# Performance work log

Measured on AMD Instinct MI355X. Metric: run time of the kernel, lower is better.

The kernel has to match this reference:

```python
import jax, jax.numpy as jnp
import numpy as np

NEG_SLOPE = 0.2

def setup_inputs() -> dict:
    key = jax.random.key(0)
    k1, k2, k3, k4, k5 = jax.random.split(key, 5)
    B, N, Fin, Fout, H = 4, 2048, 256, 128, 4
    h = jax.random.normal(k1, (B, N, Fin), dtype=jnp.float32)
    adj = jax.random.randint(k2, (N, N), 0, 2, dtype=jnp.int32)
    W_w = jax.random.normal(k3, (Fout, Fin), dtype=jnp.float32) * (1.414 / np.sqrt(Fin))
    W_b = jax.random.normal(k4, (Fout,), dtype=jnp.float32) * 0.01
    attn_w = jax.random.normal(k5, (H, 2 * Fout), dtype=jnp.float32) * (1.414 / np.sqrt(2 * Fout))
    return {"h": h, "adj": adj, "W_w": W_w, "W_b": W_b, "attn_w": attn_w}

def reference(h, adj, W_w, W_b, attn_w):
    Fout = W_w.shape[0]
    # Wh: [B, N, Fout]
    Wh = jnp.einsum('bnf,of->bno', h, W_w) + W_b
    a_left = attn_w[:, :Fout]   # [H, Fout]
    a_right = attn_w[:, Fout:]  # [H, Fout]
    e_left = jnp.einsum('bno,ho->bhn', Wh, a_left)   # [B, H, N]
    e_right = jnp.einsum('bno,ho->bhn', Wh, a_right)  # [B, H, N]
    # additive broadcast score: [B, H, N, N]
    e = e_left[:, :, :, None] + e_right[:, :, None, :]
    e = jnp.where(e > 0, e, NEG_SLOPE * e)  # LeakyReLU(0.2)
    mask = (adj == 0)[None, None, :, :]     # [1,1,N,N] broadcast over B,H
    e = jnp.where(mask, -jnp.inf, e)
    attn = jax.nn.softmax(e, axis=-1)
    attn = jnp.where(jnp.isnan(attn), 0.0, attn)
    # h_prime: [B, H, N, Fout]
    h_prime = jnp.einsum('bhij,bjo->bhio', attn, Wh)
    out = jnp.mean(h_prime, axis=1)
    return jax.nn.relu(out)
```

## Files before the change

kernel.cpp:

```cpp
#include <hip/hip_runtime.h>
#include <stdint.h>

#define BB 4
#define NN 2048
#define FIN 256
#define FOUT 128
#define NH 4
#define NEG_SLOPE 0.2f

typedef short bf16x8 __attribute__((ext_vector_type(8)));
typedef unsigned short u16x8 __attribute__((ext_vector_type(8)));
typedef float f32x4 __attribute__((ext_vector_type(4)));
typedef unsigned long long u64;

__device__ inline float b2f(unsigned short u) {
    union { unsigned int i; float f; } x; x.i = ((unsigned int)u) << 16; return x.f;
}
__device__ inline unsigned short f2b(float f) {
    union { float f; unsigned int i; } x; x.f = f;
    unsigned int r = x.i + 0x7fffu + ((x.i >> 16) & 1u);
    return (unsigned short)(r >> 16);
}
__device__ inline unsigned short f2b_fast(float f) {
    union { float f; unsigned int i; } x; x.f = f;
    return (unsigned short)((x.i + 0x8000u) >> 16);
}
union F16U { unsigned short u; _Float16 h; };
__device__ inline float f16lo(unsigned int v) { F16U x; x.u = (unsigned short)(v & 0xffffu); return (float)x.h; }
__device__ inline float f16hi(unsigned int v) { F16U x; x.u = (unsigned short)(v >> 16); return (float)x.h; }
__device__ inline unsigned int packf16(float a, float b) {
    F16U x, y; x.h = (_Float16)a; y.h = (_Float16)b;
    return (unsigned int)x.u | ((unsigned int)y.u << 16);
}

__global__ __launch_bounds__(256) void kcvt_w(const float* __restrict__ Ww,
                                              unsigned short* __restrict__ Whi,
                                              unsigned short* __restrict__ Wlo) {
    int idx = blockIdx.x * 256 + threadIdx.x;
    float v = Ww[idx];
    unsigned short hb = f2b(v);
    Whi[idx] = hb;
    Wlo[idx] = f2b(v - b2f(hb));
}

__global__ __launch_bounds__(256) void k1_wh(
    const float* __restrict__ h, const unsigned short* __restrict__ Whi,
    const unsigned short* __restrict__ Wlo, const float* __restrict__ Wb,
    const float* __restrict__ attw, unsigned short* __restrict__ WhT,
    float2* __restrict__ ELpair, unsigned int* __restrict__ ERpk) {
    __shared__ unsigned short Ahi[16][264];
    __shared__ unsigned short Alo[16][264];
    __shared__ float whs[16][132];
    int t = threadIdx.x;
    int b = blockIdx.x >> 7;
    int n0 = (blockIdx.x & 127) * 16;
    {
        int r = t >> 4, c = (t & 15) * 16;
        const float* hp = h + ((size_t)(b * NN + n0 + r)) * FIN + c;
        u16x8 hi0, hi1, lo0, lo1;
        #pragma unroll
        for (int q = 0; q < 4; ++q) {
            float4 v = *(const float4*)(hp + q * 4);
            float vv[4] = {v.x, v.y, v.z, v.w};
            #pragma unroll
            for (int e = 0; e < 4; ++e) {
                int idx = q * 4 + e;
                unsigned short hb = f2b(vv[e]);
                unsigned short lb = f2b(vv[e] - b2f(hb));
                if (idx < 8) { hi0[idx] = (short)hb; lo0[idx] = (short)lb; }
                else         { hi1[idx - 8] = (short)hb; lo1[idx - 8] = (short)lb; }
            }
        }
        *(u16x8*)&Ahi[r][c] = *(u16x8*)&hi0;
        *(u16x8*)&Ahi[r][c + 8] = *(u16x8*)&hi1;
        *(u16x8*)&Alo[r][c] = *(u16x8*)&lo0;
        *(u16x8*)&Alo[r][c + 8] = *(u16x8*)&lo1;
    }
    __syncthreads();
    int lane = t & 63, wv = t >> 6;
    int m = lane & 15, quad = lane >> 4;
    int o0 = wv * 32;
    f32x4 acc0 = {0.f, 0.f, 0.f, 0.f}, acc1 = {0.f, 0.f, 0.f, 0.f};
    const unsigned short* wh0 = Whi + (size_t)(o0 + m) * FIN;
    const unsigned short* wl0 = Wlo + (size_t)(o0 + m) * FIN;
    const unsigned short* wh1 = Whi + (size_t)(o0 + 16 + m) * FIN;
    const unsigned short* wl1 = Wlo + (size_t)(o0 + 16 + m) * FIN;
    #pragma unroll
    for (int ks = 0; ks < 8; ++ks) {
        int ko = ks * 32 + quad * 8;
        bf16x8 ahi = *(bf16x8*)&Ahi[m][ko];
        bf16x8 alo = *(bf16x8*)&Alo[m][ko];
        bf16x8 bh0 = *(const bf16x8*)(wh0 + ko);
        bf16x8 bl0 = *(const bf16x8*)(wl0 + ko);
        bf16x8 bh1 = *(const bf16x8*)(wh1 + ko);
        bf16x8 bl1 = *(const bf16x8*)(wl1 + ko);
        acc0 = __builtin_amdgcn_mfma_f32_16x16x32_bf16(ahi, bh0, acc0, 0, 0, 0);
        acc0 = __builtin_amdgcn_mfma_f32_16x16x32_bf16(ahi, bl0, acc0, 0, 0, 0);
        acc0 = __builtin_amdgcn_mfma_f32_16x16x32_bf16(alo, bh0, acc0, 0, 0, 0);
        acc1 = __builtin_amdgcn_mfma_f32_16x16x32_bf16(ahi, bh1, acc1, 0, 0, 0);
        acc1 = __builtin_amdgcn_mfma_f32_16x16x32_bf16(ahi, bl1, acc1, 0, 0, 0);
        acc1 = __builtin_amdgcn_mfma_f32_16x16x32_bf16(alo, bh1, acc1, 0, 0, 0);
    }
    float bias0 = Wb[o0 + m], bias1 = Wb[o0 + 16 + m];
    #pragma unroll
    for (int reg = 0; reg < 4; ++reg) {
        int row = quad * 4 + reg;
        whs[row][o0 + m] = acc0[reg] + bias0;
        whs[row][o0 + 16 + m] = acc1[reg] + bias1;
    }
    __syncthreads();
    {
        int o = t >> 1, half = t & 1;
        u16x8 v8;
        #pragma unroll
        for (int r = 0; r < 8; ++r) v8[r] = (short)f2b(whs[half * 8 + r][o]);
        *(u16x8*)(WhT + (size_t)(b * FOUT + o) * NN + n0 + half * 8) = v8;
    }
    {
        int outi = t >> 1, half = t & 1;
        int i = outi >> 3, d = outi & 7, hh = d & 3, side = d >> 2;
        const float* arow = attw + hh * (2 * FOUT) + side * FOUT + half * 64;
        float s = 0.f;
        #pragma unroll 8
        for (int k = 0; k < 64; ++k) s = fmaf(whs[i][half * 64 + k], arow[k], s);
        s += __shfl_xor(s, 1);
        if (half == 0) {
            float p = __expf(s), n = __expf(NEG_SLOPE * s);
            if (side == 0) {
                ELpair[(size_t)(b * NH + hh) * NN + n0 + i] = make_float2(p, n);
            } else {
                ERpk[((size_t)b * NN + n0 + i) * NH + hh] = packf16(p, n);
            }
        }
    }
}

__global__ __launch_bounds__(256) void k_pack(const int* __restrict__ adj,
                                              u64* __restrict__ mask) {
    int row = blockIdx.x;
    int wave = threadIdx.x >> 6, lane = threadIdx.x & 63;
    #pragma unroll
    for (int it = 0; it < 8; ++it) {
        int w = it * 4 + wave;
        int j = w * 64 + lane;
        u64 m = __ballot(adj[(size_t)row * NN + j] != 0);
        if (lane == 0) mask[row * 32 + w] = m;
    }
}

__global__ __launch_bounds__(256) void kstat_t(
    const unsigned int* __restrict__ ERpk, const float2* __restrict__ ELpair,
    const u64* __restrict__ mask, float* __restrict__ sPartT) {
    int lane = threadIdx.x & 63, b = threadIdx.x >> 6;
    int i = blockIdx.x * 64 + lane;
    int j0 = blockIdx.y * 64;
    u64 mw = mask[(size_t)i * 32 + (j0 >> 6)];
    float elp[NH], eln[NH], acc[NH];
    #pragma unroll
    for (int hh = 0; hh < NH; ++hh) {
        float2 e2 = ELpair[(size_t)(b * NH + hh) * NN + i];
        elp[hh] = e2.x; eln[hh] = e2.y; acc[hh] = 0.f;
    }
    const uint4* erb = (const uint4*)(ERpk + ((size_t)b * NN + j0) * NH);
    #pragma unroll 8
    for (int jj = 0; jj < 64; ++jj) {
        uint4 er4 = erb[jj];
        bool bit = (mw >> jj) & 1ull;
        float m0 = fmaxf(elp[0] * f16lo(er4.x), eln[0] * f16hi(er4.x));
        float m1 = fmaxf(elp[1] * f16lo(er4.y), eln[1] * f16hi(er4.y));
        float m2 = fmaxf(elp[2] * f16lo(er4.z), eln[2] * f16hi(er4.z));
        float m3 = fmaxf(elp[3] * f16lo(er4.w), eln[3] * f16hi(er4.w));
        acc[0] += bit ? m0 : 0.f;
        acc[1] += bit ? m1 : 0.f;
        acc[2] += bit ? m2 : 0.f;
        acc[3] += bit ? m3 : 0.f;
    }
    #pragma unroll
    for (int hh = 0; hh < NH; ++hh)
        sPartT[(((size_t)blockIdx.y * BB + b) * NH + hh) * NN + i] = acc[hh];
}

__global__ __launch_bounds__(512, 4) void k2b_mfma(
    const unsigned short* __restrict__ WhT, const unsigned int* __restrict__ ERpk,
    const float2* __restrict__ ELpair, const float* __restrict__ sPartT,
    const u64* __restrict__ mask, float* __restrict__ P) {
    __shared__ unsigned short wt[64][264];
    __shared__ u64 mws[64][8];
    __shared__ float elsc_s[64][8];
    int t = threadIdx.x;
    int b = blockIdx.y, i0 = blockIdx.x * 64, jq = blockIdx.z;
    int lane = t & 63, wv = t >> 6;
    int m = lane & 15, quad = lane >> 4;
    if (t < 256) {
        int li = t & 63, hh = t >> 6;
        float s = 0.f;
        #pragma unroll
        for (int jp = 0; jp < 32; ++jp)
            s += sPartT[(((size_t)jp * BB + b) * NH + hh) * NN + i0 + li];
        float iv = (s > 0.f) ? 0.25f / s : 0.f;
        float2 e2 = ELpair[(size_t)(b * NH + hh) * NN + i0 + li];
        elsc_s[li][hh * 2]     = e2.x * iv;
        elsc_s[li][hh * 2 + 1] = e2.y * iv;
    }
    {
        int r = t >> 3, wp = t & 7;
        mws[r][wp] = mask[(size_t)(i0 + r) * 32 + jq * 8 + wp];
    }
    int r0 = wv * 8;
    int o0 = wv * 16;
    const unsigned short* bp = WhT + (size_t)(b * FOUT + o0 + m) * NN + jq * 512;
    f32x4 acc[4];
    #pragma unroll
    for (int k = 0; k < 4; ++k) acc[k] = (f32x4){0.f, 0.f, 0.f, 0.f};

    for (int ch = 0; ch < 2; ++ch) {
        int j0 = ch * 256;
        __syncthreads();
        bf16x8 bfr[8];
        #pragma unroll
        for (int ks = 0; ks < 8; ++ks)
            bfr[ks] = *(const bf16x8*)(bp + j0 + ks * 32 + quad * 8);
        float erp[4][4], ern[4][4];
        #pragma unroll
        for (int q = 0; q < 4; ++q) {
            int jg = jq * 512 + j0 + q * 64 + lane;
            uint4 er4 = *(const uint4*)(ERpk + ((size_t)b * NN + jg) * 4);
            erp[q][0] = f16lo(er4.x); ern[q][0] = f16hi(er4.x);
            erp[q][1] = f16lo(er4.y); ern[q][1] = f16hi(er4.y);
            erp[q][2] = f16lo(er4.z); ern[q][2] = f16hi(er4.z);
            erp[q][3] = f16lo(er4.w); ern[q][3] = f16hi(er4.w);
        }
        #pragma unroll
        for (int r = 0; r < 8; ++r) {
            int ir = r0 + r;
            float4 c0 = *(float4*)&elsc_s[ir][0];
            float4 c1 = *(float4*)&elsc_s[ir][4];
            u64 mwq[4] = {mws[ir][ch * 4 + 0], mws[ir][ch * 4 + 1],
                          mws[ir][ch * 4 + 2], mws[ir][ch * 4 + 3]};
            #pragma unroll
            for (int q = 0; q < 4; ++q) {
                float p = fmaxf(c0.x * erp[q][0], c0.y * ern[q][0]);
                p += fmaxf(c0.z * erp[q][1], c0.w * ern[q][1]);
                p += fmaxf(c1.x * erp[q][2], c1.y * ern[q][2]);
                p += fmaxf(c1.z * erp[q][3], c1.w * ern[q][3]);
                wt[ir][q * 64 + lane] = ((mwq[q] >> lane) & 1ull) ? f2b_fast(p) : 0;
            }
        }
        __syncthreads();
        #pragma unroll
        for (int isub = 0; isub < 4; ++isub) {
            #pragma unroll
            for (int ks = 0; ks < 8; ++ks) {
                bf16x8 a = *(bf16x8*)&wt[isub * 16 + m][ks * 32 + quad * 8];
                acc[isub] = __builtin_amdgcn_mfma_f32_16x16x32_bf16(a, bfr[ks], acc[isub], 0, 0, 0);
            }
        }
    }
    float* pb = P + (((size_t)jq * BB + b) * NN + i0) * FOUT;
    #pragma unroll
    for (int isub = 0; isub < 4; ++isub) {
        #pragma unroll
        for (int reg = 0; reg < 4; ++reg) {
            int row = isub * 16 + quad * 4 + reg;
            pb[(size_t)row * FOUT + o0 + m] = acc[isub][reg];
        }
    }
}

__global__ __launch_bounds__(256) void k3_relu(const float* __restrict__ P,
                                               float* __restrict__ out) {
    int idx = blockIdx.x * 256 + threadIdx.x;
    const int slab = BB * NN * FOUT / 4;
    float4 a = ((const float4*)P)[idx];
    float4 c1 = ((const float4*)P)[idx + slab];
    float4 c2 = ((const float4*)P)[idx + 2 * slab];
    float4 c3 = ((const float4*)P)[idx + 3 * slab];
    a.x = fmaxf(a.x + c1.x + c2.x + c3.x, 0.f);
    a.y = fmaxf(a.y + c1.y + c2.y + c3.y, 0.f);
    a.z = fmaxf(a.z + c1.z + c2.z + c3.z, 0.f);
    a.w = fmaxf(a.w + c1.w + c2.w + c3.w, 0.f);
    ((float4*)out)[idx] = a;
}

extern "C" void kernel_launch(void* const* d_in, const int* in_sizes, int n_in,
                              void* d_out, int out_size, void* d_ws, size_t ws_size,
                              hipStream_t stream) {
    const float* h    = (const float*)d_in[0];
    const int* adj    = (const int*)d_in[1];
    const float* Ww   = (const float*)d_in[2];
    const float* Wb   = (const float*)d_in[3];
    const float* attw = (const float*)d_in[4];
    float* out = (float*)d_out;
    char* ws = (char*)d_ws;
    unsigned short* Whi = (unsigned short*)(ws);
    unsigned short* Wlo = (unsigned short*)(ws + 65536);
    unsigned short* WhT = (unsigned short*)(ws + 131072);
    float2*       ELpair = (float2*)(ws + 2228224);
    unsigned int* ERpk   = (unsigned int*)(ws + 2490368);
    u64*          mask   = (u64*)(ws + 2621440);
    float*        sPartT = (float*)(ws + 3145728);
    float*        P      = (float*)(ws + 7340032);

    kcvt_w<<<dim3(128), dim3(256), 0, stream>>>(Ww, Whi, Wlo);
    k1_wh<<<dim3(BB * NN / 16), dim3(256), 0, stream>>>(h, Whi, Wlo, Wb, attw,
                                                        WhT, ELpair, ERpk);
    k_pack<<<dim3(NN), dim3(256), 0, stream>>>(adj, mask);
    kstat_t<<<dim3(NN / 64, NN / 64), dim3(256), 0, stream>>>(ERpk, ELpair, mask, sPartT);
    k2b_mfma<<<dim3(NN / 64, BB, 4), dim3(512), 0, stream>>>(WhT, ERpk, ELpair,
                                                             sPartT, mask, P);
    k3_relu<<<dim3(BB * NN * FOUT / 1024), dim3(256), 0, stream>>>(P, out);
}
```

Baseline: 132.1 us.

## Fuse mask packing with weight conversion and fold final reduction into MFMA kernel

Merges the adjacency bit-packing and the weight hi/lo split into a single init kernel, cutting one launch. The final split-K sum plus ReLU moves into the MFMA kernel: each block increments an atomic counter, and the last of the four j-quarter blocks reads the other partials and writes the output, which removes the separate reduce kernel and one full pass over P. The shared weight tile is double-buffered by chunk, so one barrier per chunk is dropped. The cost is a memset, atomics, threadfences, a serial tail in the last block, and twice the LDS, which may lower occupancy.

```diff
diff --git a/kernel.cpp b/kernel.cpp
--- a/kernel.cpp
+++ b/kernel.cpp
@@ -33,14 +33,28 @@
     return (unsigned int)x.u | ((unsigned int)y.u << 16);
 }
 
-__global__ __launch_bounds__(256) void kcvt_w(const float* __restrict__ Ww,
-                                              unsigned short* __restrict__ Whi,
-                                              unsigned short* __restrict__ Wlo) {
-    int idx = blockIdx.x * 256 + threadIdx.x;
-    float v = Ww[idx];
-    unsigned short hb = f2b(v);
-    Whi[idx] = hb;
-    Wlo[idx] = f2b(v - b2f(hb));
+__global__ __launch_bounds__(256) void k_init(
+    const int* __restrict__ adj, const float* __restrict__ Ww,
+    u64* __restrict__ mask, unsigned short* __restrict__ Whi,
+    unsigned short* __restrict__ Wlo) {
+    int bx = blockIdx.x;
+    if (bx >= NN) {
+        int idx = (bx - NN) * 256 + threadIdx.x;
+        float v = Ww[idx];
+        unsigned short hb = f2b(v);
+        Whi[idx] = hb;
+        Wlo[idx] = f2b(v - b2f(hb));
+        return;
+    }
+    int row = bx;
+    int wave = threadIdx.x >> 6, lane = threadIdx.x & 63;
+    #pragma unroll
+    for (int it = 0; it < 8; ++it) {
+        int w = it * 4 + wave;
+        int j = w * 64 + lane;
+        u64 m = __ballot(adj[(size_t)row * NN + j] != 0);
+        if (lane == 0) mask[row * 32 + w] = m;
+    }
 }
 
 __global__ __launch_bounds__(256) void k1_wh(
@@ -135,19 +149,6 @@
     }
 }
 
-__global__ __launch_bounds__(256) void k_pack(const int* __restrict__ adj,
-                                              u64* __restrict__ mask) {
-    int row = blockIdx.x;
-    int wave = threadIdx.x >> 6, lane = threadIdx.x & 63;
-    #pragma unroll
-    for (int it = 0; it < 8; ++it) {
-        int w = it * 4 + wave;
-        int j = w * 64 + lane;
-        u64 m = __ballot(adj[(size_t)row * NN + j] != 0);
-        if (lane == 0) mask[row * 32 + w] = m;
-    }
-}
-
 __global__ __launch_bounds__(256) void kstat_t(
     const unsigned int* __restrict__ ERpk, const float2* __restrict__ ELpair,
     const u64* __restrict__ mask, float* __restrict__ sPartT) {
@@ -183,10 +184,12 @@
 __global__ __launch_bounds__(512, 4) void k2b_mfma(
     const unsigned short* __restrict__ WhT, const unsigned int* __restrict__ ERpk,
     const float2* __restrict__ ELpair, const float* __restrict__ sPartT,
-    const u64* __restrict__ mask, float* __restrict__ P) {
-    __shared__ unsigned short wt[64][264];
+    const u64* __restrict__ mask, float* __restrict__ P,
+    int* __restrict__ ctr, float* __restrict__ out) {
+    __shared__ unsigned short wt[2][64][264];
     __shared__ u64 mws[64][8];
     __shared__ float elsc_s[64][8];
+    __shared__ int lastFlag;
     int t = threadIdx.x;
     int b = blockIdx.y, i0 = blockIdx.x * 64, jq = blockIdx.z;
     int lane = t & 63, wv = t >> 6;
@@ -213,46 +216,52 @@
     #pragma unroll
     for (int k = 0; k < 4; ++k) acc[k] = (f32x4){0.f, 0.f, 0.f, 0.f};
 
+    #pragma unroll
     for (int ch = 0; ch < 2; ++ch) {
-        int j0 = ch * 256;
+        if (ch == 0) __syncthreads();
+        {
+            int j0 = ch * 256;
+            float erp[4][4], ern[4][4];
+            #pragma unroll
+            for (int q = 0; q < 4; ++q) {
+                int jg = jq * 512 + j0 + q * 64 + lane;
+                uint4 er4 = *(const uint4*)(ERpk + ((size_t)b * NN + jg) * 4);
+                erp[q][0] = f16lo(er4.x); ern[q][0] = f16hi(er4.x);
+                erp[q][1] = f16lo(er4.y); ern[q][1] = f16hi(er4.y);
+                erp[q][2] = f16lo(er4.z); ern[q][2] = f16hi(er4.z);
+                erp[q][3] = f16lo(er4.w); ern[q][3] = f16hi(er4.w);
+            }
+            #pragma unroll
+            for (int r = 0; r < 8; ++r) {
+                int ir = r0 + r;
+                float4 c0 = *(float4*)&elsc_s[ir][0];
+                float4 c1 = *(float4*)&elsc_s[ir][4];
+                u64 mwq[4] = {mws[ir][ch * 4 + 0], mws[ir][ch * 4 + 1],
+                              mws[ir][ch * 4 + 2], mws[ir][ch * 4 + 3]};
+                #pragma unroll
+                for (int q = 0; q < 4; ++q) {
+                    float p = fmaxf(c0.x * erp[q][0], c0.y * ern[q][0]);
+                    p += fmaxf(c0.z * erp[q][1], c0.w * ern[q][1]);
+                    p += fmaxf(c1.x * erp[q][2], c1.y * ern[q][2]);
+                    p += fmaxf(c1.z * erp[q][3], c1.w * ern[q][3]);
+                    wt[ch][ir][q * 64 + lane] = ((mwq[q] >> lane) & 1ull) ? f2b_fast(p) : 0;
+                }
+            }
+        }
         __syncthreads();
-        bf16x8 bfr[8];
-        #pragma unroll
-        for (int ks = 0; ks < 8; ++ks)
-            bfr[ks] = *(const bf16x8*)(bp + j0 + ks * 32 + quad * 8);
-        float erp[4][4], ern[4][4];
-        #pragma unroll
-        for (int q = 0; q < 4; ++q) {
-            int jg = jq * 512 + j0 + q * 64 + lane;
-            uint4 er4 = *(const uint4*)(ERpk + ((size_t)b * NN + jg) * 4);
-            erp[q][0] = f16lo(er4.x); ern[q][0] = f16hi(er4.x);
-            erp[q][1] = f16lo(er4.y); ern[q][1] = f16hi(er4.y);
-            erp[q][2] = f16lo(er4.z); ern[q][2] = f16hi(er4.z);
-            erp[q][3] = f16lo(er4.w); ern[q][3] = f16hi(er4.w);
-        }
-        #pragma unroll
-        for (int r = 0; r < 8; ++r) {
-            int ir = r0 + r;
-            float4 c0 = *(float4*)&elsc_s[ir][0];
-            float4 c1 = *(float4*)&elsc_s[ir][4];
-            u64 mwq[4] = {mws[ir][ch * 4 + 0], mws[ir][ch * 4 + 1],
-                          mws[ir][ch * 4 + 2], mws[ir][ch * 4 + 3]};
-            #pragma unroll
-            for (int q = 0; q < 4; ++q) {
-                float p = fmaxf(c0.x * erp[q][0], c0.y * ern[q][0]);
-                p += fmaxf(c0.z * erp[q][1], c0.w * ern[q][1]);
-                p += fmaxf(c1.x * erp[q][2], c1.y * ern[q][2]);
-                p += fmaxf(c1.z * erp[q][3], c1.w * ern[q][3]);
-                wt[ir][q * 64 + lane] = ((mwq[q] >> lane) & 1ull) ? f2b_fast(p) : 0;
-            }
-        }
-        __syncthreads();
-        #pragma unroll
-        for (int isub = 0; isub < 4; ++isub) {
-            #pragma unroll
-            for (int ks = 0; ks < 8; ++ks) {
-                bf16x8 a = *(bf16x8*)&wt[isub * 16 + m][ks * 32 + quad * 8];
-                acc[isub] = __builtin_amdgcn_mfma_f32_16x16x32_bf16(a, bfr[ks], acc[isub], 0, 0, 0);
+        {
+            int j0 = ch * 256;
+            bf16x8 bfr[8];
+            #pragma unroll
+            for (int ks = 0; ks < 8; ++ks)
+                bfr[ks] = *(const bf16x8*)(bp + j0 + ks * 32 + quad * 8);
+            #pragma unroll
+            for (int isub = 0; isub < 4; ++isub) {
+                #pragma unroll
+                for (int ks = 0; ks < 8; ++ks) {
+                    bf16x8 a = *(bf16x8*)&wt[ch][isub * 16 + m][ks * 32 + quad * 8];
+                    acc[isub] = __builtin_amdgcn_mfma_f32_16x16x32_bf16(a, bfr[ks], acc[isub], 0, 0, 0);
+                }
             }
         }
     }
@@ -265,21 +274,29 @@
             pb[(size_t)row * FOUT + o0 + m] = acc[isub][reg];
         }
     }
-}
-
-__global__ __launch_bounds__(256) void k3_relu(const float* __restrict__ P,
-                                               float* __restrict__ out) {
-    int idx = blockIdx.x * 256 + threadIdx.x;
-    const int slab = BB * NN * FOUT / 4;
-    float4 a = ((const float4*)P)[idx];
-    float4 c1 = ((const float4*)P)[idx + slab];
-    float4 c2 = ((const float4*)P)[idx + 2 * slab];
-    float4 c3 = ((const float4*)P)[idx + 3 * slab];
-    a.x = fmaxf(a.x + c1.x + c2.x + c3.x, 0.f);
-    a.y = fmaxf(a.y + c1.y + c2.y + c3.y, 0.f);
-    a.z = fmaxf(a.z + c1.z + c2.z + c3.z, 0.f);
-    a.w = fmaxf(a.w + c1.w + c2.w + c3.w, 0.f);
-    ((float4*)out)[idx] = a;
+    __threadfence();
+    if (t == 0) {
+        int old = atomicAdd(&ctr[b * 32 + blockIdx.x], 1);
+        lastFlag = (old == 3);
+    }
+    __syncthreads();
+    if (lastFlag) {
+        __threadfence();
+        #pragma unroll
+        for (int isub = 0; isub < 4; ++isub) {
+            #pragma unroll
+            for (int reg = 0; reg < 4; ++reg) {
+                int row = isub * 16 + quad * 4 + reg;
+                float v = acc[isub][reg];
+                #pragma unroll
+                for (int oq = 0; oq < 4; ++oq) {
+                    if (oq == jq) continue;
+                    v += P[(((size_t)oq * BB + b) * NN + i0 + row) * FOUT + o0 + m];
+                }
+                out[((size_t)b * NN + i0 + row) * FOUT + o0 + m] = fmaxf(v, 0.f);
+            }
+        }
+    }
 }
 
 extern "C" void kernel_launch(void* const* d_in, const int* in_sizes, int n_in,
@@ -300,13 +317,13 @@
     u64*          mask   = (u64*)(ws + 2621440);
     float*        sPartT = (float*)(ws + 3145728);
     float*        P      = (float*)(ws + 7340032);
-
-    kcvt_w<<<dim3(128), dim3(256), 0, stream>>>(Ww, Whi, Wlo);
+    int*          ctr    = (int*)(ws + 24117248);
+
+    hipMemsetAsync(ctr, 0, 512, stream);
+    k_init<<<dim3(NN + 128), dim3(256), 0, stream>>>(adj, Ww, mask, Whi, Wlo);
     k1_wh<<<dim3(BB * NN / 16), dim3(256), 0, stream>>>(h, Whi, Wlo, Wb, attw,
                                                         WhT, ELpair, ERpk);
-    k_pack<<<dim3(NN), dim3(256), 0, stream>>>(adj, mask);
     kstat_t<<<dim3(NN / 64, NN / 64), dim3(256), 0, stream>>>(ERpk, ELpair, mask, sPartT);
     k2b_mfma<<<dim3(NN / 64, BB, 4), dim3(512), 0, stream>>>(WhT, ERpk, ELpair,
-                                                             sPartT, mask, P);
-    k3_relu<<<dim3(BB * NN * FOUT / 1024), dim3(256), 0, stream>>>(P, out);
-}
+                                                             sPartT, mask, P, ctr, out);
+}
```

After: 277.2 us. 110% more time.
